# Performance work log

Hardware: AMD Instinct MI355X
Metric: run time of the kernel (lower is better)

The kernel has to match this reference:

```python
import jax, jax.numpy as jnp
import numpy as np

HID = 128
N_BATCH = 16384


def gru_cell(x, h, Wih, Whh, bih, bhh):
    # PyTorch GRUCell: weight_ih [3H, in], weight_hh [3H, H], gate order r,z,n
    gi = x @ Wih.T + bih            # [N, 3H]
    gh = h @ Whh.T + bhh            # [N, 3H]
    ir, iz, ic = jnp.split(gi, 3, axis=-1)
    hr, hz, hc = jnp.split(gh, 3, axis=-1)
    r = jax.nn.sigmoid(ir + hr)
    z = jax.nn.sigmoid(iz + hz)
    c = jnp.tanh(ic + r * hc)
    return (1.0 - z) * c + z * h


def setup_inputs() -> dict:
    key = jax.random.key(0)
    ks = jax.random.split(key, 11)
    s = 0.05  # small init like uniform(-1/sqrt(H), 1/sqrt(H))
    return {
        "x": jax.random.normal(ks[0], (N_BATCH, 1, 28, 28), jnp.float32),
        "Wih1": jax.random.normal(ks[1], (3 * HID, 28), jnp.float32) * s,
        "Whh1": jax.random.normal(ks[2], (3 * HID, HID), jnp.float32) * s,
        "bih1": jax.random.normal(ks[3], (3 * HID,), jnp.float32) * s,
        "bhh1": jax.random.normal(ks[4], (3 * HID,), jnp.float32) * s,
        "Wih2": jax.random.normal(ks[5], (3 * HID, HID), jnp.float32) * s,
        "Whh2": jax.random.normal(ks[6], (3 * HID, HID), jnp.float32) * s,
        "bih2": jax.random.normal(ks[7], (3 * HID,), jnp.float32) * s,
        "bhh2": jax.random.normal(ks[8], (3 * HID,), jnp.float32) * s,
        "Wout": jax.random.normal(ks[9], (10, HID), jnp.float32) * s,
        "bout": jax.random.normal(ks[10], (10,), jnp.float32) * s,
    }


def reference(x, Wih1, Whh1, bih1, bhh1, Wih2, Whh2, bih2, bhh2, Wout, bout):
    n, c, h, w = x.shape
    xs = x.transpose(0, 2, 1, 3).reshape(n, h, w * c)  # [N, T=28, 28]
    xs = jnp.swapaxes(xs, 0, 1)                        # [T, N, 28]
    h1_0 = jnp.zeros((n, HID), x.dtype)
    zeros_h = jnp.zeros((n, HID), x.dtype)  # cell2 gets a fresh zero hidden each step (bug in source, kept)

    def step(h1, xt):
        h0 = jax.nn.relu(gru_cell(xt, h1, Wih1, Whh1, bih1, bhh1))
        h1_new = gru_cell(h0, zeros_h, Wih2, Whh2, bih2, bhh2)
        return h1_new, None

    h1, _ = jax.lax.scan(step, h1_0, xs)
    return h1 @ Wout.T + bout  # [N, 10]
```

## Files before the change

### kernel.cpp

```cpp
#include <hip/hip_runtime.h>
#include <hip/hip_bf16.h>
#include <stdint.h>

#define HID 128
#define NB 16384
#define TSTEPS 28
#define BN 64

typedef __attribute__((ext_vector_type(8))) short s16x8;
typedef __attribute__((ext_vector_type(4))) float f32x4;

#define H1_OFF 0
#define H0_OFF 16384
#define XT_OFF 32768
#define WI2_OFF 40960
#define SMEM_BYTES 139264

__device__ __forceinline__ unsigned int f2bfu(float f) {
  union { float f; uint32_t u; } a; a.f = f;
  uint32_t r = a.u + 0x7FFFu + ((a.u >> 16) & 1u);
  return r >> 16;
}
__device__ __forceinline__ short f2bf(float f) { return (short)f2bfu(f); }
__device__ __forceinline__ unsigned int pack2bf(float lo, float hi) {
  return f2bfu(lo) | (f2bfu(hi) << 16);
}

__device__ __forceinline__ int swzh(int row, int b) {
  return (row << 8) + (b ^ (((row ^ (row >> 2)) & 7) << 4));
}
__device__ __forceinline__ int swzx(int row, int b) {
  return (row << 6) + (b ^ (((row ^ (row >> 2)) & 3) << 4));
}

__device__ __forceinline__ float fsig(float x) {
  float e = __builtin_amdgcn_exp2f(-1.442695041f * x);
  return __builtin_amdgcn_rcpf(1.0f + e);
}
__device__ __forceinline__ float ftanh(float x) {
  float xc = fminf(fmaxf(x, -15.f), 15.f);
  float e = __builtin_amdgcn_exp2f(-2.885390082f * xc);
  float r = __builtin_amdgcn_rcpf(1.0f + e);
  return fmaf(-2.0f * e, r, 1.0f);
}

__global__ __launch_bounds__(512, 1) void gru_kernel(
    const float* __restrict__ x,
    const float* __restrict__ Wih1, const float* __restrict__ Whh1,
    const float* __restrict__ bih1, const float* __restrict__ bhh1,
    const float* __restrict__ Wih2,
    const float* __restrict__ bih2, const float* __restrict__ bhh2,
    const float* __restrict__ Wout, const float* __restrict__ bout,
    float* __restrict__ out)
{
  __shared__ char smem[SMEM_BYTES];
  const int tid = threadIdx.x;
  const int wv   = tid >> 6;
  const int lane = tid & 63;
  const int l15 = lane & 15;
  const int l16 = lane >> 4;
  const int hc0 = wv * 16;
  const int n0 = blockIdx.x * BN;

  s16x8 fw_hh1[4][3];
  s16x8 fw_ih1[3];
  const int gb0 = hc0, gb1 = 128 + hc0, gb2 = 256 + hc0;
  #pragma unroll
  for (int kf = 0; kf < 4; ++kf) {
    int kbase = kf * 32 + l16 * 8;
    #pragma unroll
    for (int cb = 0; cb < 3; ++cb) {
      int g = (cb == 0 ? gb0 : cb == 1 ? gb1 : gb2) + l15;
      const float* p1 = Whh1 + g * HID + kbase;
      const float* p2 = Wih2 + g * HID + kbase;
      s16x8 f1, f2;
      #pragma unroll
      for (int j = 0; j < 8; ++j) { f1[j] = f2bf(p1[j]); f2[j] = f2bf(p2[j]); }
      fw_hh1[kf][cb] = f1;
      *(s16x8*)(smem + WI2_OFF + ((wv * 12 + kf * 3 + cb) << 10) + lane * 16) = f2;
    }
  }
  {
    int kbase = l16 * 8;
    #pragma unroll
    for (int cb = 0; cb < 3; ++cb) {
      int g = (cb == 0 ? gb0 : cb == 1 ? gb1 : gb2) + l15;
      s16x8 f;
      #pragma unroll
      for (int j = 0; j < 8; ++j) {
        int k = kbase + j;
        f[j] = (k < 28) ? f2bf(Wih1[g * 28 + k]) : (short)0;
      }
      fw_ih1[cb] = f;
    }
  }
  const float b_r  = bih1[gb0 + l15] + bhh1[gb0 + l15];
  const float b_z  = bih1[gb1 + l15] + bhh1[gb1 + l15];
  const float b_ci = bih1[gb2 + l15];
  const float b_ch = bhh1[gb2 + l15];
  const float c_r2 = bih2[gb0 + l15] + bhh2[gb0 + l15];
  const float c_z2 = bih2[gb1 + l15] + bhh2[gb1 + l15];
  const float c_c2 = bih2[gb2 + l15];
  const float c_hc2 = bhh2[gb2 + l15];

  float h1reg[4][4];
  #pragma unroll
  for (int rf = 0; rf < 4; ++rf)
    #pragma unroll
    for (int j = 0; j < 4; ++j) h1reg[rf][j] = 0.f;

  const int srow = tid >> 4, skp = tid & 15;
  {
    float2 v0 = make_float2(0.f, 0.f), v1 = make_float2(0.f, 0.f);
    if (skp < 14) {
      v0 = *(const float2*)(x + (size_t)(n0 + srow) * 784 + 2 * skp);
      v1 = *(const float2*)(x + (size_t)(n0 + srow + 32) * 784 + 2 * skp);
    }
    *(unsigned int*)(smem + XT_OFF + swzx(srow, skp * 4))      = pack2bf(v0.x, v0.y);
    *(unsigned int*)(smem + XT_OFF + swzx(srow + 32, skp * 4)) = pack2bf(v1.x, v1.y);
  }
  ((int4*)(smem + H1_OFF))[tid] = make_int4(0, 0, 0, 0);
  ((int4*)(smem + H1_OFF))[tid + 512] = make_int4(0, 0, 0, 0);
  __syncthreads();

  #pragma unroll 1
  for (int t = 0; t < TSTEPS; ++t) {
    const int xb = t & 1;
    #pragma unroll
    for (int rf = 0; rf < 4; ++rf) {
      int arow = rf * 16 + l15;
      s16x8 ax = *(const s16x8*)(smem + XT_OFF + xb * 4096 + swzx(arow, l16 * 16));
      s16x8 ah[4];
      #pragma unroll
      for (int kf = 0; kf < 4; ++kf)
        ah[kf] = *(const s16x8*)(smem + H1_OFF + swzh(arow, kf * 64 + l16 * 16));
      f32x4 aR  = {b_r,  b_r,  b_r,  b_r };
      f32x4 aZ  = {b_z,  b_z,  b_z,  b_z };
      f32x4 aCi = {b_ci, b_ci, b_ci, b_ci};
      f32x4 aCh = {b_ch, b_ch, b_ch, b_ch};
      aR  = __builtin_amdgcn_mfma_f32_16x16x32_bf16(ax, fw_ih1[0], aR, 0, 0, 0);
      aZ  = __builtin_amdgcn_mfma_f32_16x16x32_bf16(ax, fw_ih1[1], aZ, 0, 0, 0);
      aCi = __builtin_amdgcn_mfma_f32_16x16x32_bf16(ax, fw_ih1[2], aCi, 0, 0, 0);
      #pragma unroll
      for (int kf = 0; kf < 4; ++kf) {
        aR  = __builtin_amdgcn_mfma_f32_16x16x32_bf16(ah[kf], fw_hh1[kf][0], aR, 0, 0, 0);
        aZ  = __builtin_amdgcn_mfma_f32_16x16x32_bf16(ah[kf], fw_hh1[kf][1], aZ, 0, 0, 0);
        aCh = __builtin_amdgcn_mfma_f32_16x16x32_bf16(ah[kf], fw_hh1[kf][2], aCh, 0, 0, 0);
      }
      #pragma unroll
      for (int j = 0; j < 4; ++j) {
        float r = fsig(aR[j]);
        float z = fsig(aZ[j]);
        float c = ftanh(fmaf(r, aCh[j], aCi[j]));
        float h0 = fmaxf(fmaf(z, h1reg[rf][j] - c, c), 0.f);
        int row = rf * 16 + l16 * 4 + j;
        *(short*)(smem + H0_OFF + swzh(row, (hc0 + l15) << 1)) = f2bf(h0);
      }
    }
    __syncthreads();

    float2 xv0 = make_float2(0.f, 0.f), xv1 = make_float2(0.f, 0.f);
    const bool do_stage = (t + 1 < TSTEPS);
    if (do_stage && skp < 14) {
      xv0 = *(const float2*)(x + (size_t)(n0 + srow) * 784 + (t + 1) * 28 + 2 * skp);
      xv1 = *(const float2*)(x + (size_t)(n0 + srow + 32) * 784 + (t + 1) * 28 + 2 * skp);
    }
    #pragma unroll
    for (int rfh = 0; rfh < 2; ++rfh) {
      const int r0 = rfh * 32 + l15;
      const int r1 = r0 + 16;
      f32x4 aR2[2], aZ2[2], aC2[2];
      #pragma unroll
      for (int p = 0; p < 2; ++p) {
        aR2[p] = (f32x4){c_r2, c_r2, c_r2, c_r2};
        aZ2[p] = (f32x4){c_z2, c_z2, c_z2, c_z2};
        aC2[p] = (f32x4){c_c2, c_c2, c_c2, c_c2};
      }
      #pragma unroll
      for (int kf = 0; kf < 4; ++kf) {
        s16x8 a0 = *(const s16x8*)(smem + H0_OFF + swzh(r0, kf * 64 + l16 * 16));
        s16x8 a1 = *(const s16x8*)(smem + H0_OFF + swzh(r1, kf * 64 + l16 * 16));
        const char* wb = smem + WI2_OFF + ((wv * 12 + kf * 3) << 10) + lane * 16;
        s16x8 b0 = *(const s16x8*)(wb);
        s16x8 b1 = *(const s16x8*)(wb + 1024);
        s16x8 b2 = *(const s16x8*)(wb + 2048);
        aR2[0] = __builtin_amdgcn_mfma_f32_16x16x32_bf16(a0, b0, aR2[0], 0, 0, 0);
        aR2[1] = __builtin_amdgcn_mfma_f32_16x16x32_bf16(a1, b0, aR2[1], 0, 0, 0);
        aZ2[0] = __builtin_amdgcn_mfma_f32_16x16x32_bf16(a0, b1, aZ2[0], 0, 0, 0);
        aZ2[1] = __builtin_amdgcn_mfma_f32_16x16x32_bf16(a1, b1, aZ2[1], 0, 0, 0);
        aC2[0] = __builtin_amdgcn_mfma_f32_16x16x32_bf16(a0, b2, aC2[0], 0, 0, 0);
        aC2[1] = __builtin_amdgcn_mfma_f32_16x16x32_bf16(a1, b2, aC2[1], 0, 0, 0);
      }
      #pragma unroll
      for (int p = 0; p < 2; ++p)
        #pragma unroll
        for (int j = 0; j < 4; ++j) {
          float r2 = fsig(aR2[p][j]);
          float z2 = fsig(aZ2[p][j]);
          float c2 = ftanh(fmaf(r2, c_hc2, aC2[p][j]));
          float h1n = c2 - z2 * c2;
          int rf = rfh * 2 + p;
          h1reg[rf][j] = h1n;
          int row = rf * 16 + l16 * 4 + j;
          *(short*)(smem + H1_OFF + swzh(row, (hc0 + l15) << 1)) = f2bf(h1n);
        }
    }
    if (do_stage) {
      *(unsigned int*)(smem + XT_OFF + (xb ^ 1) * 4096 + swzx(srow, skp * 4)) =
          pack2bf(xv0.x, xv0.y);
      *(unsigned int*)(smem + XT_OFF + (xb ^ 1) * 4096 + swzx(srow + 32, skp * 4)) =
          pack2bf(xv1.x, xv1.y);
    }
    __syncthreads();
  }

  float* houtf = (float*)smem;
  #pragma unroll
  for (int rf = 0; rf < 4; ++rf)
    #pragma unroll
    for (int j = 0; j < 4; ++j) {
      int row = rf * 16 + l16 * 4 + j;
      houtf[row * 132 + hc0 + l15] = h1reg[rf][j];
    }
  __syncthreads();
  for (int task = tid; task < BN * 10; task += 512) {
    int row = task & 63;
    int o = task >> 6;
    const float* hp = houtf + row * 132;
    const float* wp = Wout + o * HID;
    float s = bout[o];
    #pragma unroll 8
    for (int j2 = 0; j2 < HID; ++j2) s = fmaf(hp[j2], wp[j2], s);
    out[(size_t)(n0 + row) * 10 + o] = s;
  }
}

extern "C" void kernel_launch(void* const* d_in, const int* in_sizes, int n_in,
                              void* d_out, int out_size, void* d_ws, size_t ws_size,
                              hipStream_t stream) {
  const float* x    = (const float*)d_in[0];
  const float* Wih1 = (const float*)d_in[1];
  const float* Whh1 = (const float*)d_in[2];
  const float* bih1 = (const float*)d_in[3];
  const float* bhh1 = (const float*)d_in[4];
  const float* Wih2 = (const float*)d_in[5];
  const float* bih2 = (const float*)d_in[7];
  const float* bhh2 = (const float*)d_in[8];
  const float* Wout = (const float*)d_in[9];
  const float* bout = (const float*)d_in[10];
  gru_kernel<<<NB / BN, 512, 0, stream>>>(x, Wih1, Whh1, bih1, bhh1,
                                          Wih2, bih2, bhh2, Wout, bout,
                                          (float*)d_out);
}
```

Measured before the change: 153.0 us.

## Replace XOR swizzle with padded LDS strides and use hardware bf16 pack converts

Shared-memory tiles for the hidden states and inputs now use padded row strides (272 and 80 bytes) instead of XOR swizzles. Read and write addresses become precomputed base offsets plus constants, which removes per-access index arithmetic. Software bf16 rounding is replaced by v_cvt_pk_bf16_f32, and gate biases are folded into the exp2 argument while the MFMA accumulators start from zero. The tanh clamp is dropped and the x pointers are advanced incrementally; the extra padding raises the LDS footprint slightly.

```diff
diff --git a/kernel.cpp b/kernel.cpp
--- a/kernel.cpp
+++ b/kernel.cpp
@@ -11,37 +11,30 @@
 typedef __attribute__((ext_vector_type(4))) float f32x4;
 
 #define H1_OFF 0
-#define H0_OFF 16384
-#define XT_OFF 32768
-#define WI2_OFF 40960
-#define SMEM_BYTES 139264
-
-__device__ __forceinline__ unsigned int f2bfu(float f) {
-  union { float f; uint32_t u; } a; a.f = f;
-  uint32_t r = a.u + 0x7FFFu + ((a.u >> 16) & 1u);
-  return r >> 16;
-}
-__device__ __forceinline__ short f2bf(float f) { return (short)f2bfu(f); }
-__device__ __forceinline__ unsigned int pack2bf(float lo, float hi) {
-  return f2bfu(lo) | (f2bfu(hi) << 16);
-}
-
-__device__ __forceinline__ int swzh(int row, int b) {
-  return (row << 8) + (b ^ (((row ^ (row >> 2)) & 7) << 4));
-}
-__device__ __forceinline__ int swzx(int row, int b) {
-  return (row << 6) + (b ^ (((row ^ (row >> 2)) & 3) << 4));
-}
-
-__device__ __forceinline__ float fsig(float x) {
-  float e = __builtin_amdgcn_exp2f(-1.442695041f * x);
+#define H0_OFF 17408
+#define XT_OFF 34816
+#define WI2_OFF 45056
+#define SMEM_BYTES 143360
+#define HSTRIDE 272
+#define RFSTRIDE 4352
+#define XSTRIDE 80
+
+#define L2E 1.442695041f
+#define TL2E 2.885390082f
+
+__device__ __forceinline__ unsigned cvtpk2(float lo, float hi) {
+  unsigned r;
+  asm("v_cvt_pk_bf16_f32 %0, %1, %2" : "=v"(r) : "v"(lo), "v"(hi));
+  return r;
+}
+__device__ __forceinline__ float sig_pre(float acc, float nb) {
+  float e = __builtin_amdgcn_exp2f(fmaf(acc, -L2E, nb));
   return __builtin_amdgcn_rcpf(1.0f + e);
 }
-__device__ __forceinline__ float ftanh(float x) {
-  float xc = fminf(fmaxf(x, -15.f), 15.f);
-  float e = __builtin_amdgcn_exp2f(-2.885390082f * xc);
-  float r = __builtin_amdgcn_rcpf(1.0f + e);
-  return fmaf(-2.0f * e, r, 1.0f);
+__device__ __forceinline__ float tanh_nc(float x) {
+  float e2 = __builtin_amdgcn_exp2f(x * TL2E);
+  float q = __builtin_amdgcn_rcpf(1.0f + e2);
+  return fmaf(-2.0f, q, 1.0f);
 }
 
 __global__ __launch_bounds__(512, 1) void gru_kernel(
@@ -62,6 +55,16 @@
   const int hc0 = wv * 16;
   const int n0 = blockIdx.x * BN;
 
+  f32x4 zq = {0.f, 0.f, 0.f, 0.f};
+  asm("" : "+v"(zq));
+
+  const int hrd = l15 * HSTRIDE + l16 * 16;
+  const int hwr = (4 * l16) * HSTRIDE + (hc0 + l15) * 2;
+  const int srow = tid >> 4, skp = tid & 15;
+  const int xrd = XT_OFF + l15 * XSTRIDE + l16 * 16;
+  const int xwr = XT_OFF + srow * XSTRIDE + skp * 4;
+  const int wib = WI2_OFF + wv * 12288 + lane * 16;
+
   s16x8 fw_hh1[4][3];
   s16x8 fw_ih1[3];
   const int gb0 = hc0, gb1 = 128 + hc0, gb2 = 256 + hc0;
@@ -75,9 +78,14 @@
       const float* p2 = Wih2 + g * HID + kbase;
       s16x8 f1, f2;
       #pragma unroll
-      for (int j = 0; j < 8; ++j) { f1[j] = f2bf(p1[j]); f2[j] = f2bf(p2[j]); }
+      for (int j = 0; j < 8; j += 2) {
+        unsigned u1 = cvtpk2(p1[j], p1[j + 1]);
+        unsigned u2 = cvtpk2(p2[j], p2[j + 1]);
+        f1[j] = (short)u1; f1[j + 1] = (short)(u1 >> 16);
+        f2[j] = (short)u2; f2[j + 1] = (short)(u2 >> 16);
+      }
       fw_hh1[kf][cb] = f1;
-      *(s16x8*)(smem + WI2_OFF + ((wv * 12 + kf * 3 + cb) << 10) + lane * 16) = f2;
+      *(s16x8*)(smem + wib + (kf * 3 + cb) * 1024) = f2;
     }
   }
   {
@@ -89,18 +97,18 @@
       #pragma unroll
       for (int j = 0; j < 8; ++j) {
         int k = kbase + j;
-        f[j] = (k < 28) ? f2bf(Wih1[g * 28 + k]) : (short)0;
+        f[j] = (k < 28) ? (short)cvtpk2(Wih1[g * 28 + k], 0.f) : (short)0;
       }
       fw_ih1[cb] = f;
     }
   }
-  const float b_r  = bih1[gb0 + l15] + bhh1[gb0 + l15];
-  const float b_z  = bih1[gb1 + l15] + bhh1[gb1 + l15];
-  const float b_ci = bih1[gb2 + l15];
-  const float b_ch = bhh1[gb2 + l15];
-  const float c_r2 = bih2[gb0 + l15] + bhh2[gb0 + l15];
-  const float c_z2 = bih2[gb1 + l15] + bhh2[gb1 + l15];
-  const float c_c2 = bih2[gb2 + l15];
+  const float nb_r  = -L2E * (bih1[gb0 + l15] + bhh1[gb0 + l15]);
+  const float nb_z  = -L2E * (bih1[gb1 + l15] + bhh1[gb1 + l15]);
+  const float b_ci  = bih1[gb2 + l15];
+  const float b_ch  = bhh1[gb2 + l15];
+  const float nb_r2 = -L2E * (bih2[gb0 + l15] + bhh2[gb0 + l15]);
+  const float nb_z2 = -L2E * (bih2[gb1 + l15] + bhh2[gb1 + l15]);
+  const float c_c2  = bih2[gb2 + l15];
   const float c_hc2 = bhh2[gb2 + l15];
 
   float h1reg[4][4];
@@ -109,107 +117,117 @@
     #pragma unroll
     for (int j = 0; j < 4; ++j) h1reg[rf][j] = 0.f;
 
-  const int srow = tid >> 4, skp = tid & 15;
+  const float2* xp0 = (const float2*)(x + (size_t)(n0 + srow) * 784 + 2 * skp);
+  const float2* xp1 = (const float2*)(x + (size_t)(n0 + srow + 32) * 784 + 2 * skp);
+
   {
     float2 v0 = make_float2(0.f, 0.f), v1 = make_float2(0.f, 0.f);
-    if (skp < 14) {
-      v0 = *(const float2*)(x + (size_t)(n0 + srow) * 784 + 2 * skp);
-      v1 = *(const float2*)(x + (size_t)(n0 + srow + 32) * 784 + 2 * skp);
-    }
-    *(unsigned int*)(smem + XT_OFF + swzx(srow, skp * 4))      = pack2bf(v0.x, v0.y);
-    *(unsigned int*)(smem + XT_OFF + swzx(srow + 32, skp * 4)) = pack2bf(v1.x, v1.y);
-  }
-  ((int4*)(smem + H1_OFF))[tid] = make_int4(0, 0, 0, 0);
-  ((int4*)(smem + H1_OFF))[tid + 512] = make_int4(0, 0, 0, 0);
+    if (skp < 14) { v0 = *xp0; v1 = *xp1; }
+    xp0 += 14; xp1 += 14;
+    *(unsigned*)(smem + xwr)        = cvtpk2(v0.x, v0.y);
+    *(unsigned*)(smem + xwr + 2560) = cvtpk2(v1.x, v1.y);
+  }
+  #pragma unroll
+  for (int i = 0; i < 3; ++i) {
+    int idx = tid + i * 512;
+    if (idx < 1088) ((int4*)(smem + H1_OFF))[idx] = make_int4(0, 0, 0, 0);
+  }
   __syncthreads();
 
   #pragma unroll 1
   for (int t = 0; t < TSTEPS; ++t) {
-    const int xb = t & 1;
+    const int xb = (t & 1) * 5120;
     #pragma unroll
     for (int rf = 0; rf < 4; ++rf) {
-      int arow = rf * 16 + l15;
-      s16x8 ax = *(const s16x8*)(smem + XT_OFF + xb * 4096 + swzx(arow, l16 * 16));
+      s16x8 ax = *(const s16x8*)(smem + xrd + xb + rf * 1280);
       s16x8 ah[4];
       #pragma unroll
       for (int kf = 0; kf < 4; ++kf)
-        ah[kf] = *(const s16x8*)(smem + H1_OFF + swzh(arow, kf * 64 + l16 * 16));
-      f32x4 aR  = {b_r,  b_r,  b_r,  b_r };
-      f32x4 aZ  = {b_z,  b_z,  b_z,  b_z };
-      f32x4 aCi = {b_ci, b_ci, b_ci, b_ci};
-      f32x4 aCh = {b_ch, b_ch, b_ch, b_ch};
-      aR  = __builtin_amdgcn_mfma_f32_16x16x32_bf16(ax, fw_ih1[0], aR, 0, 0, 0);
-      aZ  = __builtin_amdgcn_mfma_f32_16x16x32_bf16(ax, fw_ih1[1], aZ, 0, 0, 0);
-      aCi = __builtin_amdgcn_mfma_f32_16x16x32_bf16(ax, fw_ih1[2], aCi, 0, 0, 0);
+        ah[kf] = *(const s16x8*)(smem + H1_OFF + hrd + rf * RFSTRIDE + kf * 64);
+      f32x4 aR, aZ, aCi, aCh;
+      aR  = __builtin_amdgcn_mfma_f32_16x16x32_bf16(ax, fw_ih1[0], zq, 0, 0, 0);
+      aZ  = __builtin_amdgcn_mfma_f32_16x16x32_bf16(ax, fw_ih1[1], zq, 0, 0, 0);
+      aCi = __builtin_amdgcn_mfma_f32_16x16x32_bf16(ax, fw_ih1[2], zq, 0, 0, 0);
+      aCh = __builtin_amdgcn_mfma_f32_16x16x32_bf16(ah[0], fw_hh1[0][2], zq, 0, 0, 0);
       #pragma unroll
       for (int kf = 0; kf < 4; ++kf) {
-        aR  = __builtin_amdgcn_mfma_f32_16x16x32_bf16(ah[kf], fw_hh1[kf][0], aR, 0, 0, 0);
-        aZ  = __builtin_amdgcn_mfma_f32_16x16x32_bf16(ah[kf], fw_hh1[kf][1], aZ, 0, 0, 0);
-        aCh = __builtin_amdgcn_mfma_f32_16x16x32_bf16(ah[kf], fw_hh1[kf][2], aCh, 0, 0, 0);
-      }
+        aR = __builtin_amdgcn_mfma_f32_16x16x32_bf16(ah[kf], fw_hh1[kf][0], aR, 0, 0, 0);
+        aZ = __builtin_amdgcn_mfma_f32_16x16x32_bf16(ah[kf], fw_hh1[kf][1], aZ, 0, 0, 0);
+        if (kf > 0)
+          aCh = __builtin_amdgcn_mfma_f32_16x16x32_bf16(ah[kf], fw_hh1[kf][2], aCh, 0, 0, 0);
+      }
+      float h0v[4];
       #pragma unroll
       for (int j = 0; j < 4; ++j) {
-        float r = fsig(aR[j]);
-        float z = fsig(aZ[j]);
-        float c = ftanh(fmaf(r, aCh[j], aCi[j]));
-        float h0 = fmaxf(fmaf(z, h1reg[rf][j] - c, c), 0.f);
-        int row = rf * 16 + l16 * 4 + j;
-        *(short*)(smem + H0_OFF + swzh(row, (hc0 + l15) << 1)) = f2bf(h0);
-      }
+        float r = sig_pre(aR[j], nb_r);
+        float z = sig_pre(aZ[j], nb_z);
+        float c = tanh_nc(fmaf(r, aCh[j] + b_ch, aCi[j] + b_ci));
+        h0v[j] = fmaxf(fmaf(z, h1reg[rf][j] - c, c), 0.f);
+      }
+      unsigned pk01 = cvtpk2(h0v[0], h0v[1]);
+      unsigned pk23 = cvtpk2(h0v[2], h0v[3]);
+      *(short*)(smem + H0_OFF + hwr + rf * RFSTRIDE + 0 * HSTRIDE) = (short)pk01;
+      *(short*)(smem + H0_OFF + hwr + rf * RFSTRIDE + 1 * HSTRIDE) = (short)(pk01 >> 16);
+      *(short*)(smem + H0_OFF + hwr + rf * RFSTRIDE + 2 * HSTRIDE) = (short)pk23;
+      *(short*)(smem + H0_OFF + hwr + rf * RFSTRIDE + 3 * HSTRIDE) = (short)(pk23 >> 16);
     }
     __syncthreads();
 
     float2 xv0 = make_float2(0.f, 0.f), xv1 = make_float2(0.f, 0.f);
     const bool do_stage = (t + 1 < TSTEPS);
-    if (do_stage && skp < 14) {
-      xv0 = *(const float2*)(x + (size_t)(n0 + srow) * 784 + (t + 1) * 28 + 2 * skp);
-      xv1 = *(const float2*)(x + (size_t)(n0 + srow + 32) * 784 + (t + 1) * 28 + 2 * skp);
-    }
+    if (do_stage && skp < 14) { xv0 = *xp0; xv1 = *xp1; }
+    xp0 += 14; xp1 += 14;
     #pragma unroll
     for (int rfh = 0; rfh < 2; ++rfh) {
-      const int r0 = rfh * 32 + l15;
-      const int r1 = r0 + 16;
       f32x4 aR2[2], aZ2[2], aC2[2];
       #pragma unroll
+      for (int kf = 0; kf < 4; ++kf) {
+        s16x8 a0 = *(const s16x8*)(smem + H0_OFF + hrd + rfh * 8704 + kf * 64);
+        s16x8 a1 = *(const s16x8*)(smem + H0_OFF + hrd + rfh * 8704 + RFSTRIDE + kf * 64);
+        s16x8 b0 = *(const s16x8*)(smem + wib + (kf * 3 + 0) * 1024);
+        s16x8 b1 = *(const s16x8*)(smem + wib + (kf * 3 + 1) * 1024);
+        s16x8 b2 = *(const s16x8*)(smem + wib + (kf * 3 + 2) * 1024);
+        if (kf == 0) {
+          aR2[0] = __builtin_amdgcn_mfma_f32_16x16x32_bf16(a0, b0, zq, 0, 0, 0);
+          aR2[1] = __builtin_amdgcn_mfma_f32_16x16x32_bf16(a1, b0, zq, 0, 0, 0);
+          aZ2[0] = __builtin_amdgcn_mfma_f32_16x16x32_bf16(a0, b1, zq, 0, 0, 0);
+          aZ2[1] = __builtin_amdgcn_mfma_f32_16x16x32_bf16(a1, b1, zq, 0, 0, 0);
+          aC2[0] = __builtin_amdgcn_mfma_f32_16x16x32_bf16(a0, b2, zq, 0, 0, 0);
+          aC2[1] = __builtin_amdgcn_mfma_f32_16x16x32_bf16(a1, b2, zq, 0, 0, 0);
+        } else {
+          aR2[0] = __builtin_amdgcn_mfma_f32_16x16x32_bf16(a0, b0, aR2[0], 0, 0, 0);
+          aR2[1] = __builtin_amdgcn_mfma_f32_16x16x32_bf16(a1, b0, aR2[1], 0, 0, 0);
+          aZ2[0] = __builtin_amdgcn_mfma_f32_16x16x32_bf16(a0, b1, aZ2[0], 0, 0, 0);
+          aZ2[1] = __builtin_amdgcn_mfma_f32_16x16x32_bf16(a1, b1, aZ2[1], 0, 0, 0);
+          aC2[0] = __builtin_amdgcn_mfma_f32_16x16x32_bf16(a0, b2, aC2[0], 0, 0, 0);
+          aC2[1] = __builtin_amdgcn_mfma_f32_16x16x32_bf16(a1, b2, aC2[1], 0, 0, 0);
+        }
+      }
+      #pragma unroll
       for (int p = 0; p < 2; ++p) {
-        aR2[p] = (f32x4){c_r2, c_r2, c_r2, c_r2};
-        aZ2[p] = (f32x4){c_z2, c_z2, c_z2, c_z2};
-        aC2[p] = (f32x4){c_c2, c_c2, c_c2, c_c2};
-      }
-      #pragma unroll
-      for (int kf = 0; kf < 4; ++kf) {
-        s16x8 a0 = *(const s16x8*)(smem + H0_OFF + swzh(r0, kf * 64 + l16 * 16));
-        s16x8 a1 = *(const s16x8*)(smem + H0_OFF + swzh(r1, kf * 64 + l16 * 16));
-        const char* wb = smem + WI2_OFF + ((wv * 12 + kf * 3) << 10) + lane * 16;
-        s16x8 b0 = *(const s16x8*)(wb);
-        s16x8 b1 = *(const s16x8*)(wb + 1024);
-        s16x8 b2 = *(const s16x8*)(wb + 2048);
-        aR2[0] = __builtin_amdgcn_mfma_f32_16x16x32_bf16(a0, b0, aR2[0], 0, 0, 0);
-        aR2[1] = __builtin_amdgcn_mfma_f32_16x16x32_bf16(a1, b0, aR2[1], 0, 0, 0);
-        aZ2[0] = __builtin_amdgcn_mfma_f32_16x16x32_bf16(a0, b1, aZ2[0], 0, 0, 0);
-        aZ2[1] = __builtin_amdgcn_mfma_f32_16x16x32_bf16(a1, b1, aZ2[1], 0, 0, 0);
-        aC2[0] = __builtin_amdgcn_mfma_f32_16x16x32_bf16(a0, b2, aC2[0], 0, 0, 0);
-        aC2[1] = __builtin_amdgcn_mfma_f32_16x16x32_bf16(a1, b2, aC2[1], 0, 0, 0);
-      }
-      #pragma unroll
-      for (int p = 0; p < 2; ++p)
+        const int rf = rfh * 2 + p;
+        float hv[4];
         #pragma unroll
         for (int j = 0; j < 4; ++j) {
-          float r2 = fsig(aR2[p][j]);
-          float z2 = fsig(aZ2[p][j]);
-          float c2 = ftanh(fmaf(r2, c_hc2, aC2[p][j]));
-          float h1n = c2 - z2 * c2;
-          int rf = rfh * 2 + p;
+          float r2 = sig_pre(aR2[p][j], nb_r2);
+          float z2 = sig_pre(aZ2[p][j], nb_z2);
+          float c2 = tanh_nc(fmaf(r2, c_hc2, aC2[p][j] + c_c2));
+          float h1n = fmaf(-z2, c2, c2);
           h1reg[rf][j] = h1n;
-          int row = rf * 16 + l16 * 4 + j;
-          *(short*)(smem + H1_OFF + swzh(row, (hc0 + l15) << 1)) = f2bf(h1n);
+          hv[j] = h1n;
         }
+        unsigned pk01 = cvtpk2(hv[0], hv[1]);
+        unsigned pk23 = cvtpk2(hv[2], hv[3]);
+        *(short*)(smem + H1_OFF + hwr + rf * RFSTRIDE + 0 * HSTRIDE) = (short)pk01;
+        *(short*)(smem + H1_OFF + hwr + rf * RFSTRIDE + 1 * HSTRIDE) = (short)(pk01 >> 16);
+        *(short*)(smem + H1_OFF + hwr + rf * RFSTRIDE + 2 * HSTRIDE) = (short)pk23;
+        *(short*)(smem + H1_OFF + hwr + rf * RFSTRIDE + 3 * HSTRIDE) = (short)(pk23 >> 16);
+      }
     }
     if (do_stage) {
-      *(unsigned int*)(smem + XT_OFF + (xb ^ 1) * 4096 + swzx(srow, skp * 4)) =
-          pack2bf(xv0.x, xv0.y);
-      *(unsigned int*)(smem + XT_OFF + (xb ^ 1) * 4096 + swzx(srow + 32, skp * 4)) =
-          pack2bf(xv1.x, xv1.y);
+      const int xo = 5120 - xb;
+      *(unsigned*)(smem + xwr + xo)        = cvtpk2(xv0.x, xv0.y);
+      *(unsigned*)(smem + xwr + xo + 2560) = cvtpk2(xv1.x, xv1.y);
     }
     __syncthreads();
   }
```

After: 154.4 us. About the same (+0.9%).
